# Optimization experiments

Measured on AMD Instinct MI355X. Metric: run time of the kernel, lower is better.

Reference implementation:

```python
import jax, jax.numpy as jnp
import numpy as np

N_ATOMS = 10000
N_EDGES = 200000
L_MAX = 2
K_L = [32, 24, 16]  # k_max_l = n_element_channels * n_max_l

# (l1, l2, L) in the original loop order (l1 outer, l2 inner, L ascending)
PAIRS = [(0,0,0),(0,1,1),(0,2,2),
         (1,0,1),(1,1,0),(1,1,1),(1,1,2),(1,2,1),(1,2,2),
         (2,0,2),(2,1,1),(2,1,2),(2,2,0),(2,2,1),(2,2,2)]
# concatenated input width -> k_max_l[L] per (L, sigma) channel
LIN = {'0_1': (72, 32), '1_1': (80, 24), '1_m1': (40, 24), '2_1': (72, 16), '2_m1': (32, 16)}


def setup_inputs() -> dict:
    key = jax.random.key(0)
    it = iter(jax.random.split(key, 64))
    def nrm(shape):
        return jax.random.normal(next(it), shape, dtype=jnp.float32)
    inp = {}
    for l in range(L_MAX + 1):
        inp['rb%d' % l] = nrm((N_EDGES, K_L[l]))           # radial basis per l
    for l in range(L_MAX + 1):
        inp['sh%d' % l] = nrm((N_EDGES, 2*l+1, 1))         # spherical harmonics per l
    inp['emb'] = nrm((N_ATOMS, 1, K_L[0]))                 # initial center embedding
    for l in range(L_MAX + 1):
        inp['f%d' % l] = nrm((N_ATOMS, 2*l+1, K_L[l]))     # nu=1 equivariant features
    for (l1, l2, L) in PAIRS:
        inp['cg_%d_%d_%d' % (l1, l2, L)] = nrm(((2*l1+1)*(2*l2+1), 2*L+1))
    for LS, (fin, fout) in LIN.items():
        inp['W_' + LS] = nrm((fin, fout)) / np.float32(np.sqrt(fin))
        inp['b_' + LS] = nrm((fout,)) * 0.01
    inp['centers'] = jax.random.randint(next(it), (N_EDGES,), 0, N_ATOMS)
    inp['neighbors'] = jax.random.randint(next(it), (N_EDGES,), 0, N_ATOMS)
    inp['n_atoms'] = N_ATOMS
    return inp


def _normalize(x, dims):
    # Normalizer(dims): RMS normalization over the given dims
    return x * jax.lax.rsqrt(jnp.mean(x * x, axis=dims, keepdims=True) + 1e-12)


def _forward(floats, centers, neighbors, n_atoms):
    (rb0, rb1, rb2, sh0, sh1, sh2, emb, f0, f1, f2,
     cg_0_0_0, cg_0_1_1, cg_0_2_2, cg_1_0_1, cg_1_1_0, cg_1_1_1, cg_1_1_2,
     cg_1_2_1, cg_1_2_2, cg_2_0_2, cg_2_1_1, cg_2_1_2, cg_2_2_0, cg_2_2_1,
     cg_2_2_2, W_0_1, b_0_1, W_1_1, b_1_1, W_1_m1, b_1_m1, W_2_1, b_2_1,
     W_2_m1, b_2_m1) = floats
    rb = [rb0, rb1, rb2]; sh = [sh0, sh1, sh2]; feats = [f0, f1, f2]
    cgs = {'0_0_0': cg_0_0_0, '0_1_1': cg_0_1_1, '0_2_2': cg_0_2_2,
           '1_0_1': cg_1_0_1, '1_1_0': cg_1_1_0, '1_1_1': cg_1_1_1,
           '1_1_2': cg_1_1_2, '1_2_1': cg_1_2_1, '1_2_2': cg_1_2_2,
           '2_0_2': cg_2_0_2, '2_1_1': cg_2_1_1, '2_1_2': cg_2_1_2,
           '2_2_0': cg_2_2_0, '2_2_1': cg_2_2_1, '2_2_2': cg_2_2_2}
    lin = {'0_1': (W_0_1, b_0_1), '1_1': (W_1_1, b_1_1), '1_m1': (W_1_m1, b_1_m1),
           '2_1': (W_2_1, b_2_1), '2_m1': (W_2_m1, b_2_m1)}

    # ---- InvariantMessagePasser: density_l = scatter_add over centers of
    #      sh_l * rb_l * emb[neighbors]
    emb_n = emb[neighbors]                                       # [E, 1, k0]
    densities = []
    for l in range(L_MAX + 1):
        msg = sh[l] * rb[l][:, None, :] * emb_n[:, :, :K_L[l]]   # [E, 2l+1, k_l]
        densities.append(jax.ops.segment_sum(msg, centers, num_segments=n_atoms))

    # ---- EquivariantMessagePasser
    ve = [sh[l] * rb[l][:, None, :] for l in range(L_MAX + 1)]   # vector expansion [E,2l+1,k_l]
    fn = [feats[l][neighbors] for l in range(L_MAX + 1)]         # gathered neighbor feats
    results = {}
    for (l1, l2, L) in PAIRS:
        S = (-1) ** (l1 + l2 + L)
        k = min(K_L[l1], K_L[l2])
        t1 = ve[l1][:, :, :k]                                    # [E, 2l1+1, k]
        t2 = fn[l2][:, :, :k]                                    # [E, 2l2+1, k]
        cg = cgs['%d_%d_%d' % (l1, l2, L)].reshape(2*l1+1, 2*l2+1, 2*L+1)
        # fused outer product + CG contraction -> [E, 2L+1, k]
        res = jnp.einsum('eak,ebk,abM->eMk', t1, t2, cg)
        pooled = jax.ops.segment_sum(res, centers, num_segments=n_atoms)
        LS = '%d_%s' % (L, 'm1' if S < 0 else '1')
        results.setdefault(LS, []).append(pooled)

    outs = {}
    for LS, (W, b) in lin.items():
        x = jnp.concatenate(results[LS], axis=2)                 # [n_atoms, 2L+1, size_LS]
        x = _normalize(x, (0, 1))
        x = jnp.einsum('amf,fk->amk', x, W) + b
        outs[LS] = _normalize(x, (0, 1, 2))

    return (densities[0], densities[1], densities[2],
            outs['0_1'], outs['1_1'], outs['1_m1'], outs['2_1'], outs['2_m1'])


def reference(rb0, rb1, rb2, sh0, sh1, sh2, emb, f0, f1, f2,
              cg_0_0_0, cg_0_1_1, cg_0_2_2, cg_1_0_1, cg_1_1_0, cg_1_1_1,
              cg_1_1_2, cg_1_2_1, cg_1_2_2, cg_2_0_2, cg_2_1_1, cg_2_1_2,
              cg_2_2_0, cg_2_2_1, cg_2_2_2, W_0_1, b_0_1, W_1_1, b_1_1,
              W_1_m1, b_1_m1, W_2_1, b_2_1, W_2_m1, b_2_m1,
              centers, neighbors, n_atoms):
    floats = (rb0, rb1, rb2, sh0, sh1, sh2, emb, f0, f1, f2,
              cg_0_0_0, cg_0_1_1, cg_0_2_2, cg_1_0_1, cg_1_1_0, cg_1_1_1,
              cg_1_1_2, cg_1_2_1, cg_1_2_2, cg_2_0_2, cg_2_1_1, cg_2_1_2,
              cg_2_2_0, cg_2_2_1, cg_2_2_2, W_0_1, b_0_1, W_1_1, b_1_1,
              W_1_m1, b_1_m1, W_2_1, b_2_1, W_2_m1, b_2_m1)
    return _forward(floats, centers, neighbors, n_atoms)
```

## Files before the change

### kernel.cpp

```cpp
#include <hip/hip_runtime.h>
#include <hip/hip_bf16.h>

typedef __hip_bfloat16 bf16;

#define N_ATOMS 10000
#define N_EDGES 200000

#define SCG   0
#define SINV  616
#define SS1P  1024
#define SS2P  19968
#define SWS2  20288
#define SINTS 20352
#define IFLAG  0
#define ICOUNT 16
#define IOFFS  10016
#define ICURS  20032
#define IELIST 30032
#define INTS_END_SMALL 230032
#define INTS_END_BIG   430032
#define SXACC (SINTS + INTS_END_BIG)
#define BIG_FLOATS (SXACC + 952*N_ATOMS)

#define O0 0
#define O1 320000
#define O2 1040000
#define OY 1840000
#define OUT_ELEMS 5200000

__device__ __forceinline__ float b2f(bf16 x){ return __bfloat162float(x); }
__device__ __forceinline__ bf16  f2b(float x){ return __float2bfloat16(x); }

__device__ __forceinline__ float ldv(const float* p, int i){ return p[i]; }
__device__ __forceinline__ float ldv(const bf16*  p, int i){ return b2f(p[i]); }
__device__ __forceinline__ void  stv(float* p, int i, float v){ p[i] = v; }
__device__ __forceinline__ void  stv(bf16*  p, int i, float v){ p[i] = f2b(v); }

template<typename T> __device__ __forceinline__ int dtid();
template<> __device__ __forceinline__ int dtid<bf16>(){ return 0; }
template<> __device__ __forceinline__ int dtid<float>(){ return 1; }

struct Ptrs15 { const void* p[15]; };
struct LinP   { const void* W[5]; const void* B[5]; };

__constant__ int c_cg_sizes[15] = {1,9,25,9,9,27,45,45,75,25,45,75,25,75,125};
__constant__ int c_fin[5]   = {72,80,40,72,32};
__constant__ int c_kout[5]  = {32,24,24,16,16};
__constant__ int c_yoff[5]  = {OY+0, OY+320000, OY+1040000, OY+1760000, OY+2560000};
__constant__ int c_numel[5] = {320000,720000,720000,800000,800000};
__constant__ int c_cum[6]   = {0,32,104,176,256,336};
__constant__ int c_xb[5]    = {0,72,312,432,792};
__constant__ int c_Ms[5]    = {1,3,3,5,5};

__global__ void k_zero(float* wsf, int* wsi,
                       const unsigned short* rb0u, const unsigned short* embu) {
  if (blockIdx.x == 0 && threadIdx.x < 64) {
    int lane = threadIdx.x;
    int bad = 0;
    for (int i = lane; i < 256; i += 64) {
      unsigned u1 = ((unsigned)rb0u[2*i]) << 16;
      unsigned u2 = ((unsigned)embu[2*i]) << 16;
      float v1 = __uint_as_float(u1);
      float v2 = __uint_as_float(u2);
      if (!(fabsf(v1) < 1e9f) || !(fabsf(v2) < 1e9f)) bad = 1;
    }
    unsigned long long any = __ballot(bad);
    if (lane == 0) wsi[IFLAG] = (any != 0ULL) ? 1 : 0;
  }
  int i = blockIdx.x*blockDim.x + threadIdx.x;
  if (i < N_ATOMS) wsi[ICOUNT + i] = 0;
  int j = i - N_ATOMS;
  if (j >= 0 && j < N_ATOMS) wsi[ICURS + j] = 0;
  j -= N_ATOMS;
  if (j >= 0 && j < 18944) wsf[SS1P + j] = 0.f;
  j -= 18944;
  if (j >= 0 && j < 325) wsf[SS2P + j] = 0.f;
}

template<typename T>
__global__ void k_cg(Ptrs15 cg, float* wsf, const int* flag) {
  if (flag[0] != dtid<T>()) return;
  int i = blockIdx.x*blockDim.x + threadIdx.x;
  if (i >= 615) return;
  int s = 0, off = i;
  while (off >= c_cg_sizes[s]) { off -= c_cg_sizes[s]; ++s; }
  wsf[SCG + i] = ldv((const T*)cg.p[s], off);
}

__global__ void k_hist(const int* __restrict__ centers, int* __restrict__ counts) {
  int e = blockIdx.x*blockDim.x + threadIdx.x;
  if (e < N_EDGES) atomicAdd(&counts[centers[e]], 1);
}

__global__ void k_scan(const int* __restrict__ counts, int* __restrict__ offs) {
  __shared__ int part[1024];
  int t = threadIdx.x;
  int base = t*10;
  int s = 0;
  for (int i = 0; i < 10; ++i) { int idx = base+i; if (idx < N_ATOMS) s += counts[idx]; }
  part[t] = s;
  __syncthreads();
  for (int d = 1; d < 1024; d <<= 1) {
    int v = part[t];
    int add = (t >= d) ? part[t-d] : 0;
    __syncthreads();
    part[t] = v + add;
    __syncthreads();
  }
  int run = (t == 0) ? 0 : part[t-1];
  for (int i = 0; i < 10; ++i) {
    int idx = base+i;
    if (idx < N_ATOMS) { offs[idx] = run; run += counts[idx]; }
  }
  if (t == 1023) offs[N_ATOMS] = part[1023];
}

__global__ void k_scatter(const int* __restrict__ centers, const int* __restrict__ offs,
                          int* __restrict__ cursors, int* __restrict__ elist) {
  int e = blockIdx.x*blockDim.x + threadIdx.x;
  if (e < N_EDGES) {
    int c = centers[e];
    int p = atomicAdd(&cursors[c], 1);
    elist[offs[c] + p] = e;
  }
}

__global__ void k_scatter2(const int* __restrict__ centers, const int* __restrict__ neighbors,
                           const int* __restrict__ offs, int* __restrict__ cursors,
                           int2* __restrict__ elist2) {
  int e = blockIdx.x*blockDim.x + threadIdx.x;
  if (e < N_EDGES) {
    int c = centers[e];
    int p = atomicAdd(&cursors[c], 1);
    elist2[offs[c] + p] = make_int2(e, neighbors[e]);
  }
}

template<typename T, int MODE>
__global__ __launch_bounds__(256) void k_main(
    const T* __restrict__ rb0, const T* __restrict__ rb1, const T* __restrict__ rb2,
    const T* __restrict__ sh0, const T* __restrict__ sh1, const T* __restrict__ sh2,
    const T* __restrict__ emb, const T* __restrict__ f0, const T* __restrict__ f1,
    const T* __restrict__ f2, const int* __restrict__ neighbors,
    const int* __restrict__ offs, const int* __restrict__ elist,
    const float* __restrict__ cgf, float* __restrict__ s1p,
    const float* __restrict__ inv, float* __restrict__ s2p,
    float* __restrict__ xout, LinP lp, T* __restrict__ out,
    const int* __restrict__ flag)
{
  if (flag[0] != dtid<T>()) return;
  int lane = threadIdx.x & 63;
  int wv   = threadIdx.x >> 6;
  int tix  = threadIdx.x;
  int a = blockIdx.x;
  int beg = offs[a];
  int cnt = offs[a+1] - beg;
  int k32 = lane & 31, e2 = lane >> 5;
  int k16 = lane & 15, e4 = lane >> 4;
  const int2* el2 = (const int2*)elist;
  int ab = a & 63;

  __shared__ int2 sel[256];
  __shared__ __align__(16) float L[952];
  __shared__ float red[4][5];

  float acc[25];
  #pragma unroll
  for (int i = 0; i < 25; ++i) acc[i] = 0.f;

  for (int cbase = 0; cbase < cnt; cbase += 256) {
    int nch = cnt - cbase; if (nch > 256) nch = 256;
    __syncthreads();
    if (tix < nch) {
      if constexpr (MODE == 0) {
        sel[tix] = el2[beg + cbase + tix];
      } else {
        int e = elist[beg + cbase + tix];
        sel[tix] = make_int2(e, neighbors[e]);
      }
    }
    __syncthreads();

    if (wv == 0) {
      for (int base = 0; base < nch; base += 4) {
        #pragma unroll
        for (int u = 0; u < 2; ++u) {
          int idx = base + 2*u + e2;
          float w = (idx < nch) ? 1.f : 0.f;
          int ic  = (idx < nch) ? idx : 0;
          int2 en = sel[ic];
          int e = en.x, n = en.y;
          float s0 = ldv(sh0, e);
          float s1a0 = ldv(sh1, e*3+0), s1a1 = ldv(sh1, e*3+1), s1a2 = ldv(sh1, e*3+2);
          float rb0k = ldv(rb0, e*32 + k32) * w;
          float ek   = ldv(emb, n*32 + k32);
          float f0k  = ldv(f0,  n*32 + k32);
          float ve0 = s0 * rb0k;
          acc[0] = fmaf(ve0, ek, acc[0]);
          acc[4] = fmaf(ve0, f0k, acc[4]);
          if (k32 < 24) {
            float rb1k = ldv(rb1, e*24 + k32) * w;
            float f1k0 = ldv(f1, n*72 + k32);
            float f1k1 = ldv(f1, n*72 + 24 + k32);
            float f1k2 = ldv(f1, n*72 + 48 + k32);
            float rbek = rb1k * ek;
            acc[1] = fmaf(s1a0, rbek, acc[1]);
            acc[2] = fmaf(s1a1, rbek, acc[2]);
            acc[3] = fmaf(s1a2, rbek, acc[3]);
            acc[5] = fmaf(ve0, f1k0, acc[5]);
            acc[6] = fmaf(ve0, f1k1, acc[6]);
            acc[7] = fmaf(ve0, f1k2, acc[7]);
            float g3 = rb1k * f0k;
            acc[8]  = fmaf(g3, s1a0, acc[8]);
            acc[9]  = fmaf(g3, s1a1, acc[9]);
            acc[10] = fmaf(g3, s1a2, acc[10]);
            #pragma unroll
            for (int aa = 0; aa < 3; ++aa) {
              float sa = rb1k * ((aa==0)?s1a0:(aa==1)?s1a1:s1a2);
              acc[11+aa*3+0] = fmaf(sa, f1k0, acc[11+aa*3+0]);
              acc[11+aa*3+1] = fmaf(sa, f1k1, acc[11+aa*3+1]);
              acc[11+aa*3+2] = fmaf(sa, f1k2, acc[11+aa*3+2]);
            }
          }
        }
      }
    } else if (wv == 1) {
      for (int base = 0; base < nch; base += 8) {
        #pragma unroll
        for (int u = 0; u < 2; ++u) {
          int idx = base + 4*u + e4;
          float w = (idx < nch) ? 1.f : 0.f;
          int ic  = (idx < nch) ? idx : 0;
          int2 en = sel[ic];
          int e = en.x, n = en.y;
          float s0 = ldv(sh0, e);
          float s1a[3];
          #pragma unroll
          for (int m = 0; m < 3; ++m) s1a[m] = ldv(sh1, e*3+m);
          float s2a[5];
          #pragma unroll
          for (int m = 0; m < 5; ++m) s2a[m] = ldv(sh2, e*5+m);
          float rb0k = ldv(rb0, e*32 + k16) * w;
          float rb1k = ldv(rb1, e*24 + k16) * w;
          float rb2k = ldv(rb2, e*16 + k16) * w;
          float ek   = ldv(emb, n*32 + k16);
          float f2k[5];
          #pragma unroll
          for (int b = 0; b < 5; ++b) f2k[b] = ldv(f2, n*80 + b*16 + k16);
          float re = rb2k * ek;
          #pragma unroll
          for (int m = 0; m < 5; ++m) acc[m] = fmaf(s2a[m], re, acc[m]);
          float ve0 = s0 * rb0k;
          #pragma unroll
          for (int b = 0; b < 5; ++b) acc[5+b] = fmaf(ve0, f2k[b], acc[5+b]);
          #pragma unroll
          for (int aa = 0; aa < 3; ++aa) {
            float sa = rb1k * s1a[aa];
            #pragma unroll
            for (int b = 0; b < 5; ++b)
              acc[10+aa*5+b] = fmaf(sa, f2k[b], acc[10+aa*5+b]);
          }
        }
      }
    } else if (wv == 2) {
      for (int base = 0; base < nch; base += 8) {
        #pragma unroll
        for (int u = 0; u < 2; ++u) {
          int idx = base + 4*u + e4;
          float w = (idx < nch) ? 1.f : 0.f;
          int ic  = (idx < nch) ? idx : 0;
          int2 en = sel[ic];
          int e = en.x, n = en.y;
          float s2a[5];
          #pragma unroll
          for (int m = 0; m < 5; ++m) s2a[m] = ldv(sh2, e*5+m);
          float rb2k = ldv(rb2, e*16 + k16) * w;
          float f0k  = ldv(f0,  n*32 + k16);
          float f1k[3];
          #pragma unroll
          for (int b = 0; b < 3; ++b) f1k[b] = ldv(f1, n*72 + b*24 + k16);
          float g9 = rb2k * f0k;
          #pragma unroll
          for (int aa = 0; aa < 5; ++aa) acc[aa] = fmaf(g9, s2a[aa], acc[aa]);
          #pragma unroll
          for (int aa = 0; aa < 5; ++aa) {
            float sa = rb2k * s2a[aa];
            #pragma unroll
            for (int b = 0; b < 3; ++b)
              acc[5+aa*3+b] = fmaf(sa, f1k[b], acc[5+aa*3+b]);
          }
        }
      }
    } else {
      for (int base = 0; base < nch; base += 8) {
        #pragma unroll
        for (int u = 0; u < 2; ++u) {
          int idx = base + 4*u + e4;
          float w = (idx < nch) ? 1.f : 0.f;
          int ic  = (idx < nch) ? idx : 0;
          int2 en = sel[ic];
          int e = en.x, n = en.y;
          float s2a[5];
          #pragma unroll
          for (int m = 0; m < 5; ++m) s2a[m] = ldv(sh2, e*5+m);
          float rb2k = ldv(rb2, e*16 + k16) * w;
          float f2k[5];
          #pragma unroll
          for (int b = 0; b < 5; ++b) f2k[b] = ldv(f2, n*80 + b*16 + k16);
          #pragma unroll
          for (int aa = 0; aa < 5; ++aa) {
            float sa = rb2k * s2a[aa];
            #pragma unroll
            for (int b = 0; b < 5; ++b)
              acc[aa*5+b] = fmaf(sa, f2k[b], acc[aa*5+b]);
          }
        }
      }
    }
  }

  if (wv == 0) {
    #pragma unroll
    for (int i = 0; i < 20; ++i) acc[i] += __shfl_xor(acc[i], 32);
    const float* C000 = cgf + 0;
    const float* C011 = cgf + 1;
    const float* C101 = cgf + 35;
    const float* C110 = cgf + 44;
    const float* C111 = cgf + 53;
    const float* C112 = cgf + 80;
    float r[16];
    r[0] = C000[0] * acc[4];
    #pragma unroll
    for (int M = 0; M < 3; ++M) {
      float t = 0.f;
      #pragma unroll
      for (int b = 0; b < 3; ++b) t = fmaf(acc[5+b], C011[b*3+M], t);
      r[1+M] = t;
    }
    #pragma unroll
    for (int M = 0; M < 3; ++M) {
      float t = 0.f;
      #pragma unroll
      for (int aa = 0; aa < 3; ++aa) t = fmaf(acc[8+aa], C101[aa*3+M], t);
      r[4+M] = t;
    }
    {
      float t = 0.f;
      #pragma unroll
      for (int q = 0; q < 9; ++q) t = fmaf(acc[11+q], C110[q], t);
      r[7] = t;
    }
    #pragma unroll
    for (int M = 0; M < 3; ++M) {
      float t = 0.f;
      #pragma unroll
      for (int q = 0; q < 9; ++q) t = fmaf(acc[11+q], C111[q*3+M], t);
      r[8+M] = t;
    }
    #pragma unroll
    for (int M = 0; M < 5; ++M) {
      float t = 0.f;
      #pragma unroll
      for (int q = 0; q < 9; ++q) t = fmaf(acc[11+q], C112[q*5+M], t);
      r[11+M] = t;
    }
    acc[4] = r[0];
    #pragma unroll
    for (int M = 0; M < 3; ++M) acc[5+M]  = r[1+M];
    #pragma unroll
    for (int M = 0; M < 3; ++M) acc[8+M]  = r[4+M];
    acc[11] = r[7];
    #pragma unroll
    for (int M = 0; M < 3; ++M) acc[12+M] = r[8+M];
    #pragma unroll
    for (int M = 0; M < 5; ++M) acc[15+M] = r[11+M];
  } else if (wv == 1) {
    #pragma unroll
    for (int i = 0; i < 25; ++i) {
      acc[i] += __shfl_xor(acc[i], 16);
      acc[i] += __shfl_xor(acc[i], 32);
    }
    const float* C022 = cgf + 10;
    const float* C121 = cgf + 125;
    const float* C122 = cgf + 170;
    float r[13];
    #pragma unroll
    for (int M = 0; M < 5; ++M) {
      float t = 0.f;
      #pragma unroll
      for (int b = 0; b < 5; ++b) t = fmaf(acc[5+b], C022[b*5+M], t);
      r[M] = t;
    }
    #pragma unroll
    for (int M = 0; M < 3; ++M) {
      float t = 0.f;
      #pragma unroll
      for (int q = 0; q < 15; ++q) t = fmaf(acc[10+q], C121[q*3+M], t);
      r[5+M] = t;
    }
    #pragma unroll
    for (int M = 0; M < 5; ++M) {
      float t = 0.f;
      #pragma unroll
      for (int q = 0; q < 15; ++q) t = fmaf(acc[10+q], C122[q*5+M], t);
      r[8+M] = t;
    }
    #pragma unroll
    for (int M = 0; M < 5; ++M) acc[5+M]  = r[M];
    #pragma unroll
    for (int M = 0; M < 3; ++M) acc[10+M] = r[5+M];
    #pragma unroll
    for (int M = 0; M < 5; ++M) acc[13+M] = r[8+M];
  } else if (wv == 2) {
    #pragma unroll
    for (int i = 0; i < 20; ++i) {
      acc[i] += __shfl_xor(acc[i], 16);
      acc[i] += __shfl_xor(acc[i], 32);
    }
    const float* C202 = cgf + 245;
    const float* C211 = cgf + 270;
    const float* C212 = cgf + 315;
    float r[13];
    #pragma unroll
    for (int M = 0; M < 5; ++M) {
      float t = 0.f;
      #pragma unroll
      for (int aa = 0; aa < 5; ++aa) t = fmaf(acc[aa], C202[aa*5+M], t);
      r[M] = t;
    }
    #pragma unroll
    for (int M = 0; M < 3; ++M) {
      float t = 0.f;
      #pragma unroll
      for (int q = 0; q < 15; ++q) t = fmaf(acc[5+q], C211[q*3+M], t);
      r[5+M] = t;
    }
    #pragma unroll
    for (int M = 0; M < 5; ++M) {
      float t = 0.f;
      #pragma unroll
      for (int q = 0; q < 15; ++q) t = fmaf(acc[5+q], C212[q*5+M], t);
      r[8+M] = t;
    }
    #pragma unroll
    for (int M = 0; M < 5; ++M) acc[M]   = r[M];
    #pragma unroll
    for (int M = 0; M < 3; ++M) acc[5+M] = r[5+M];
    #pragma unroll
    for (int M = 0; M < 5; ++M) acc[8+M] = r[8+M];
  } else {
    #pragma unroll
    for (int i = 0; i < 25; ++i) {
      acc[i] += __shfl_xor(acc[i], 16);
      acc[i] += __shfl_xor(acc[i], 32);
    }
    const float* C220 = cgf + 390;
    const float* C221 = cgf + 415;
    const float* C222 = cgf + 490;
    float r[9];
    {
      float t = 0.f;
      #pragma unroll
      for (int q = 0; q < 25; ++q) t = fmaf(acc[q], C220[q], t);
      r[0] = t;
    }
    #pragma unroll
    for (int M = 0; M < 3; ++M) {
      float t = 0.f;
      #pragma unroll
      for (int q = 0; q < 25; ++q) t = fmaf(acc[q], C221[q*3+M], t);
      r[1+M] = t;
    }
    #pragma unroll
    for (int M = 0; M < 5; ++M) {
      float t = 0.f;
      #pragma unroll
      for (int q = 0; q < 25; ++q) t = fmaf(acc[q], C222[q*5+M], t);
      r[4+M] = t;
    }
    #pragma unroll
    for (int i = 0; i < 9; ++i) acc[i] = r[i];
  }

  if constexpr (MODE != 2) {
    if (wv == 0) {
      if (lane < 32) {
        stv(out, O0 + a*32 + k32, acc[0]);
        atomicAdd(&s1p[(0+k32)*64+ab], acc[4]*acc[4]);
        if (k32 < 24) {
          #pragma unroll
          for (int m = 0; m < 3; ++m) stv(out, O1 + a*72 + m*24 + k32, acc[1+m]);
          atomicAdd(&s1p[(32+k32)*64+ab], acc[11]*acc[11]);
          float q;
          q = acc[5]*acc[5]+acc[6]*acc[6]+acc[7]*acc[7];
          atomicAdd(&s1p[(72+k32)*64+ab], q);
          q = acc[8]*acc[8]+acc[9]*acc[9]+acc[10]*acc[10];
          atomicAdd(&s1p[(96+k32)*64+ab], q);
          q = acc[12]*acc[12]+acc[13]*acc[13]+acc[14]*acc[14];
          atomicAdd(&s1p[(152+k32)*64+ab], q);
          q = acc[15]*acc[15]+acc[16]*acc[16]+acc[17]*acc[17]
            + acc[18]*acc[18]+acc[19]*acc[19];
          atomicAdd(&s1p[(208+k32)*64+ab], q);
        }
      }
    } else if (wv == 1) {
      if (lane < 16) {
        #pragma unroll
        for (int m = 0; m < 5; ++m) stv(out, O2 + a*80 + m*16 + k16, acc[m]);
        float q;
        q = acc[5]*acc[5]+acc[6]*acc[6]+acc[7]*acc[7]+acc[8]*acc[8]+acc[9]*acc[9];
        atomicAdd(&s1p[(192+k16)*64+ab], q);
        q = acc[10]*acc[10]+acc[11]*acc[11]+acc[12]*acc[12];
        atomicAdd(&s1p[(120+k16)*64+ab], q);
        q = acc[13]*acc[13]+acc[14]*acc[14]+acc[15]*acc[15]
          + acc[16]*acc[16]+acc[17]*acc[17];
        atomicAdd(&s1p[(264+k16)*64+ab], q);
      }
    } else if (wv == 2) {
      if (lane < 16) {
        float q;
        q = acc[0]*acc[0]+acc[1]*acc[1]+acc[2]*acc[2]+acc[3]*acc[3]+acc[4]*acc[4];
        atomicAdd(&s1p[(232+k16)*64+ab], q);
        q = acc[5]*acc[5]+acc[6]*acc[6]+acc[7]*acc[7];
        atomicAdd(&s1p[(136+k16)*64+ab], q);
        q = acc[8]*acc[8]+acc[9]*acc[9]+acc[10]*acc[10]
          + acc[11]*acc[11]+acc[12]*acc[12];
        atomicAdd(&s1p[(280+k16)*64+ab], q);
      }
    } else {
      if (lane < 16) {
        atomicAdd(&s1p[(56+k16)*64+ab], acc[0]*acc[0]);
        float q;
        q = acc[1]*acc[1]+acc[2]*acc[2]+acc[3]*acc[3];
        atomicAdd(&s1p[(176+k16)*64+ab], q);
        q = acc[4]*acc[4]+acc[5]*acc[5]+acc[6]*acc[6]
          + acc[7]*acc[7]+acc[8]*acc[8];
        atomicAdd(&s1p[(248+k16)*64+ab], q);
      }
    }
  }

  if constexpr (MODE == 0) {
    if (wv == 0) {
      if (lane < 32) {
        L[k32] = acc[4];
        if (k32 < 24) {
          L[32+k32] = acc[11];
          #pragma unroll
          for (int M = 0; M < 3; ++M) L[72+M*80+k32]     = acc[5+M];
          #pragma unroll
          for (int M = 0; M < 3; ++M) L[72+M*80+24+k32]  = acc[8+M];
          #pragma unroll
          for (int M = 0; M < 3; ++M) L[312+M*40+k32]    = acc[12+M];
          #pragma unroll
          for (int M = 0; M < 5; ++M) L[432+M*72+16+k32] = acc[15+M];
        }
      }
    } else if (wv == 1) {
      if (lane < 16) {
        #pragma unroll
        for (int M = 0; M < 5; ++M) L[432+M*72+k16]    = acc[5+M];
        #pragma unroll
        for (int M = 0; M < 3; ++M) L[72+M*80+48+k16]  = acc[10+M];
        #pragma unroll
        for (int M = 0; M < 5; ++M) L[792+M*32+k16]    = acc[13+M];
      }
    } else if (wv == 2) {
      if (lane < 16) {
        #pragma unroll
        for (int M = 0; M < 5; ++M) L[432+M*72+40+k16] = acc[0+M];
        #pragma unroll
        for (int M = 0; M < 3; ++M) L[72+M*80+64+k16]  = acc[5+M];
        #pragma unroll
        for (int M = 0; M < 5; ++M) L[792+M*32+16+k16] = acc[8+M];
      }
    } else {
      if (lane < 16) {
        L[56+k16] = acc[0];
        #pragma unroll
        for (int M = 0; M < 3; ++M) L[312+M*40+24+k16] = acc[1+M];
        #pragma unroll
        for (int M = 0; M < 5; ++M) L[432+M*72+56+k16] = acc[4+M];
      }
    }
    __syncthreads();
    const float4* Ls = (const float4*)L;
    float4* xd = (float4*)(xout + a*952);
    for (int i = tix; i < 238; i += 256) xd[i] = Ls[i];
  }

  if constexpr (MODE == 2) {
    if (wv == 0) {
      if (lane < 32) {
        L[k32] = acc[4]*inv[k32];
        if (k32 < 24) {
          L[32+k32] = acc[11]*inv[32+k32];
          #pragma unroll
          for (int M = 0; M < 3; ++M) L[72+M*80+k32]     = acc[5+M]*inv[72+k32];
          #pragma unroll
          for (int M = 0; M < 3; ++M) L[72+M*80+24+k32]  = acc[8+M]*inv[96+k32];
          #pragma unroll
          for (int M = 0; M < 3; ++M) L[312+M*40+k32]    = acc[12+M]*inv[152+k32];
          #pragma unroll
          for (int M = 0; M < 5; ++M) L[432+M*72+16+k32] = acc[15+M]*inv[208+k32];
        }
      }
    } else if (wv == 1) {
      if (lane < 16) {
        #pragma unroll
        for (int M = 0; M < 5; ++M) L[432+M*72+k16]    = acc[5+M]*inv[192+k16];
        #pragma unroll
        for (int M = 0; M < 3; ++M) L[72+M*80+48+k16]  = acc[10+M]*inv[120+k16];
        #pragma unroll
        for (int M = 0; M < 5; ++M) L[792+M*32+k16]    = acc[13+M]*inv[264+k16];
      }
    } else if (wv == 2) {
      if (lane < 16) {
        #pragma unroll
        for (int M = 0; M < 5; ++M) L[432+M*72+40+k16] = acc[0+M]*inv[232+k16];
        #pragma unroll
        for (int M = 0; M < 3; ++M) L[72+M*80+64+k16]  = acc[5+M]*inv[136+k16];
        #pragma unroll
        for (int M = 0; M < 5; ++M) L[792+M*32+16+k16] = acc[8+M]*inv[280+k16];
      }
    } else {
      if (lane < 16) {
        L[56+k16] = acc[0]*inv[56+k16];
        #pragma unroll
        for (int M = 0; M < 3; ++M) L[312+M*40+24+k16] = acc[1+M]*inv[176+k16];
        #pragma unroll
        for (int M = 0; M < 5; ++M) L[432+M*72+56+k16] = acc[4+M]*inv[248+k16];
      }
    }
    __syncthreads();
    int t = threadIdx.x;
    float y2[5] = {0.f,0.f,0.f,0.f,0.f};
    for (int tau = t; tau < 336; tau += 256) {
      int ls = 0;
      while (tau >= c_cum[ls+1]) ++ls;
      int rem = tau - c_cum[ls];
      int kn = c_kout[ls], fin = c_fin[ls];
      int M = rem / kn, ko = rem - M*kn;
      const T* W = (const T*)lp.W[ls];
      float y = ldv((const T*)lp.B[ls], ko);
      const float* xv = &L[c_xb[ls] + M*fin];
      for (int f = 0; f < fin; ++f) y = fmaf(xv[f], ldv(W, f*kn+ko), y);
      stv(out, c_yoff[ls] + (a*c_Ms[ls] + M)*kn + ko, y);
      y2[ls] += y*y;
    }
    #pragma unroll
    for (int i = 0; i < 5; ++i) {
      y2[i] += __shfl_xor(y2[i], 1);  y2[i] += __shfl_xor(y2[i], 2);
      y2[i] += __shfl_xor(y2[i], 4);  y2[i] += __shfl_xor(y2[i], 8);
      y2[i] += __shfl_xor(y2[i], 16); y2[i] += __shfl_xor(y2[i], 32);
    }
    if (lane == 0) {
      #pragma unroll
      for (int i = 0; i < 5; ++i) red[wv][i] = y2[i];
    }
    __syncthreads();
    if (t == 0) {
      #pragma unroll
      for (int i = 0; i < 5; ++i)
        atomicAdd(&s2p[i*64 + ab], red[0][i]+red[1][i]+red[2][i]+red[3][i]);
    }
  }
}

template<typename T>
__global__ __launch_bounds__(256) void k_lin(
    const float* __restrict__ xg, const float* __restrict__ inv,
    LinP lp, T* __restrict__ out, float* __restrict__ s2p,
    const int* __restrict__ flag)
{
  if (flag[0] != dtid<T>()) return;
  int a = blockIdx.x;
  int t = threadIdx.x;
  __shared__ float L[952];
  for (int i = t; i < 952; i += 256) {
    int ch;
    if      (i < 72)  ch = i;
    else if (i < 312) ch = 72  + (i-72)  % 80;
    else if (i < 432) ch = 152 + (i-312) % 40;
    else if (i < 792) ch = 192 + (i-432) % 72;
    else              ch = 264 + (i-792) % 32;
    L[i] = xg[a*952 + i] * inv[ch];
  }
  __syncthreads();
  float y2[5] = {0.f,0.f,0.f,0.f,0.f};
  for (int tau = t; tau < 336; tau += 256) {
    int ls = 0;
    while (tau >= c_cum[ls+1]) ++ls;
    int rem = tau - c_cum[ls];
    int kn = c_kout[ls], fin = c_fin[ls];
    int M = rem / kn, ko = rem - M*kn;
    const T* W = (const T*)lp.W[ls];
    float y = ldv((const T*)lp.B[ls], ko);
    const float* xv = &L[c_xb[ls] + M*fin];
    for (int f = 0; f < fin; ++f) y = fmaf(xv[f], ldv(W, f*kn+ko), y);
    stv(out, c_yoff[ls] + (a*c_Ms[ls] + M)*kn + ko, y);
    y2[ls] += y*y;
  }
  __shared__ float red[4][5];
  #pragma unroll
  for (int i = 0; i < 5; ++i) {
    y2[i] += __shfl_xor(y2[i], 1);  y2[i] += __shfl_xor(y2[i], 2);
    y2[i] += __shfl_xor(y2[i], 4);  y2[i] += __shfl_xor(y2[i], 8);
    y2[i] += __shfl_xor(y2[i], 16); y2[i] += __shfl_xor(y2[i], 32);
  }
  if ((t & 63) == 0) {
    #pragma unroll
    for (int i = 0; i < 5; ++i) red[t>>6][i] = y2[i];
  }
  __syncthreads();
  if (t == 0) {
    #pragma unroll
    for (int i = 0; i < 5; ++i)
      atomicAdd(&s2p[i*64 + (a & 63)], red[0][i]+red[1][i]+red[2][i]+red[3][i]);
  }
}

__global__ void k_red1(const float* __restrict__ s1p, float* __restrict__ inv) {
  int ch = blockIdx.x, lane = threadIdx.x;
  float v = s1p[ch*64 + lane];
  v += __shfl_xor(v, 1);  v += __shfl_xor(v, 2);  v += __shfl_xor(v, 4);
  v += __shfl_xor(v, 8);  v += __shfl_xor(v, 16); v += __shfl_xor(v, 32);
  if (lane == 0) {
    float rows = (ch < 72) ? 10000.f : (ch < 192) ? 30000.f : 50000.f;
    inv[ch] = rsqrtf(v/rows + 1e-12f);
  }
}

__global__ void k_red2(const float* __restrict__ s2p, float* __restrict__ ws2) {
  int ls = blockIdx.x, lane = threadIdx.x;
  float v = s2p[ls*64 + lane];
  v += __shfl_xor(v, 1);  v += __shfl_xor(v, 2);  v += __shfl_xor(v, 4);
  v += __shfl_xor(v, 8);  v += __shfl_xor(v, 16); v += __shfl_xor(v, 32);
  if (lane == 0) ws2[ls] = v;
}

template<typename T>
__global__ void k_scale(const float* __restrict__ ws2, T* __restrict__ out,
                        const int* __restrict__ flag) {
  if (flag[0] != dtid<T>()) return;
  int i = blockIdx.x*blockDim.x + threadIdx.x;
  if (i >= 3360000) return;
  int ls = (i < 320000) ? 0 : (i < 1040000) ? 1 : (i < 1760000) ? 2 : (i < 2560000) ? 3 : 4;
  float scale = rsqrtf(ws2[ls] / (float)c_numel[ls] + 1e-12f);
  stv(out, OY + i, ldv((const T*)out, OY + i) * scale);
}

template<typename T>
static void launch_chain(void* const* d_in, T* out, float* wsf, int* wsi,
                         Ptrs15 cg, LinP lp, bool big, hipStream_t stream) {
  const T* rb0 = (const T*)d_in[0];
  const T* rb1 = (const T*)d_in[1];
  const T* rb2 = (const T*)d_in[2];
  const T* sh0 = (const T*)d_in[3];
  const T* sh1 = (const T*)d_in[4];
  const T* sh2 = (const T*)d_in[5];
  const T* emb = (const T*)d_in[6];
  const T* f0  = (const T*)d_in[7];
  const T* f1  = (const T*)d_in[8];
  const T* f2  = (const T*)d_in[9];
  const int* neighbors = (const int*)d_in[36];
  const int* flag = wsi + IFLAG;

  k_cg<T><<<3, 256, 0, stream>>>(cg, wsf, flag);
  if (big) {
    k_main<T,0><<<N_ATOMS, 256, 0, stream>>>(rb0, rb1, rb2, sh0, sh1, sh2, emb, f0, f1, f2,
        neighbors, wsi+IOFFS, wsi+IELIST, wsf+SCG, wsf+SS1P, nullptr, nullptr,
        wsf+SXACC, lp, out, flag);
    k_red1<<<296, 64, 0, stream>>>(wsf+SS1P, wsf+SINV);
    k_lin<T><<<N_ATOMS, 256, 0, stream>>>(wsf+SXACC, wsf+SINV, lp, out, wsf+SS2P, flag);
  } else {
    k_main<T,1><<<N_ATOMS, 256, 0, stream>>>(rb0, rb1, rb2, sh0, sh1, sh2, emb, f0, f1, f2,
        neighbors, wsi+IOFFS, wsi+IELIST, wsf+SCG, wsf+SS1P, nullptr, nullptr,
        nullptr, lp, out, flag);
    k_red1<<<296, 64, 0, stream>>>(wsf+SS1P, wsf+SINV);
    k_main<T,2><<<N_ATOMS, 256, 0, stream>>>(rb0, rb1, rb2, sh0, sh1, sh2, emb, f0, f1, f2,
        neighbors, wsi+IOFFS, wsi+IELIST, wsf+SCG, nullptr, wsf+SINV, wsf+SS2P,
        nullptr, lp, out, flag);
  }
  k_red2<<<5, 64, 0, stream>>>(wsf+SS2P, wsf+SWS2);
  k_scale<T><<<(3360000+255)/256, 256, 0, stream>>>(wsf+SWS2, out, flag);
}

extern "C" void kernel_launch(void* const* d_in, const int* in_sizes, int n_in,
                              void* d_out, int out_size, void* d_ws, size_t ws_size,
                              hipStream_t stream) {
  float* wsf = (float*)d_ws;
  int*   wsi = (int*)(wsf + SINTS);
  const int* centers   = (const int*)d_in[35];
  const int* neighbors = (const int*)d_in[36];
  bool big = ws_size >= (size_t)BIG_FLOATS * 4;

  int know = -1;
  if (in_sizes) {
    long long nb = (long long)in_sizes[0];
    if (nb == (long long)N_EDGES*32*2) know = 0;
    else if (nb == (long long)N_EDGES*32*4) know = 1;
  }
  if (know < 0) {
    long long ob = (long long)out_size;
    if (ob == (long long)OUT_ELEMS*2) know = 0;
    else if (ob == (long long)OUT_ELEMS*4) know = 1;
  }

  Ptrs15 cg;
  for (int i = 0; i < 15; ++i) cg.p[i] = d_in[10+i];
  LinP lp;
  lp.W[0] = d_in[25]; lp.B[0] = d_in[26];
  lp.W[1] = d_in[27]; lp.B[1] = d_in[28];
  lp.W[2] = d_in[29]; lp.B[2] = d_in[30];
  lp.W[3] = d_in[31]; lp.B[3] = d_in[32];
  lp.W[4] = d_in[33]; lp.B[4] = d_in[34];

  k_zero<<<154, 256, 0, stream>>>(wsf, wsi,
                                  (const unsigned short*)d_in[0],
                                  (const unsigned short*)d_in[6]);
  k_hist<<<(N_EDGES+255)/256, 256, 0, stream>>>(centers, wsi+ICOUNT);
  k_scan<<<1, 1024, 0, stream>>>(wsi+ICOUNT, wsi+IOFFS);
  if (big) {
    k_scatter2<<<(N_EDGES+255)/256, 256, 0, stream>>>(centers, neighbors, wsi+IOFFS,
                                                      wsi+ICURS, (int2*)(wsi+IELIST));
  } else {
    k_scatter<<<(N_EDGES+255)/256, 256, 0, stream>>>(centers, wsi+IOFFS, wsi+ICURS, wsi+IELIST);
  }

  if (know != 1) launch_chain<bf16 >(d_in, (bf16*)d_out,  wsf, wsi, cg, lp, big, stream);
  if (know != 0) launch_chain<float>(d_in, (float*)d_out, wsf, wsi, cg, lp, big, stream);
}
```

Measured before the change: 514.2 us.

## Stage per-edge and neighbor rows into shared memory with vectorized loads

Each block now processes edges in chunks of 32 and cooperatively copies each edge's radial basis and spherical harmonics, plus the neighbor's embedding and feature rows, into shared memory using 4-wide vector loads. The four wave-specialized loops then read from shared memory instead of issuing scattered scalar global loads per lane, and the same rows are no longer fetched separately by every wave. The int2 edge list and its scatter2 kernel are dropped, so the neighbor index is always looked up at chunk load. In exchange there are more block barriers per atom (every 32 edges instead of 256), a larger shared-memory footprint that may cut occupancy, and the v4 casts assume 16-byte (float) or 8-byte (bf16) alignment of the row offsets.

```diff
diff --git a/kernel.cpp b/kernel.cpp
--- a/kernel.cpp
+++ b/kernel.cpp
@@ -17,9 +17,8 @@
 #define IOFFS  10016
 #define ICURS  20032
 #define IELIST 30032
-#define INTS_END_SMALL 230032
-#define INTS_END_BIG   430032
-#define SXACC (SINTS + INTS_END_BIG)
+#define INTS_END 230032
+#define SXACC (SINTS + INTS_END)
 #define BIG_FLOATS (SXACC + 952*N_ATOMS)
 
 #define O0 0
@@ -35,6 +34,13 @@
 __device__ __forceinline__ float ldv(const bf16*  p, int i){ return b2f(p[i]); }
 __device__ __forceinline__ void  stv(float* p, int i, float v){ p[i] = v; }
 __device__ __forceinline__ void  stv(bf16*  p, int i, float v){ p[i] = f2b(v); }
+
+__device__ __forceinline__ void v4cp(bf16* d, const bf16* s){
+  *reinterpret_cast<ushort4*>(d) = *reinterpret_cast<const ushort4*>(s);
+}
+__device__ __forceinline__ void v4cp(float* d, const float* s){
+  *reinterpret_cast<float4*>(d) = *reinterpret_cast<const float4*>(s);
+}
 
 template<typename T> __device__ __forceinline__ int dtid();
 template<> __device__ __forceinline__ int dtid<bf16>(){ return 0; }
@@ -122,17 +128,6 @@
     int c = centers[e];
     int p = atomicAdd(&cursors[c], 1);
     elist[offs[c] + p] = e;
-  }
-}
-
-__global__ void k_scatter2(const int* __restrict__ centers, const int* __restrict__ neighbors,
-                           const int* __restrict__ offs, int* __restrict__ cursors,
-                           int2* __restrict__ elist2) {
-  int e = blockIdx.x*blockDim.x + threadIdx.x;
-  if (e < N_EDGES) {
-    int c = centers[e];
-    int p = atomicAdd(&cursors[c], 1);
-    elist2[offs[c] + p] = make_int2(e, neighbors[e]);
   }
 }
 
@@ -157,10 +152,11 @@
   int cnt = offs[a+1] - beg;
   int k32 = lane & 31, e2 = lane >> 5;
   int k16 = lane & 15, e4 = lane >> 4;
-  const int2* el2 = (const int2*)elist;
   int ab = a & 63;
 
-  __shared__ int2 sel[256];
+  __shared__ int2 sel[32];
+  __shared__ T SE[32][84];
+  __shared__ T SN[32][216];
   __shared__ __align__(16) float L[952];
   __shared__ float red[4][5];
 
@@ -168,15 +164,37 @@
   #pragma unroll
   for (int i = 0; i < 25; ++i) acc[i] = 0.f;
 
-  for (int cbase = 0; cbase < cnt; cbase += 256) {
-    int nch = cnt - cbase; if (nch > 256) nch = 256;
+  for (int cbase = 0; cbase < cnt; cbase += 32) {
+    int nch = cnt - cbase; if (nch > 32) nch = 32;
     __syncthreads();
     if (tix < nch) {
-      if constexpr (MODE == 0) {
-        sel[tix] = el2[beg + cbase + tix];
-      } else {
-        int e = elist[beg + cbase + tix];
-        sel[tix] = make_int2(e, neighbors[e]);
+      int e = elist[beg + cbase + tix];
+      sel[tix] = make_int2(e, neighbors[e]);
+    }
+    __syncthreads();
+    {
+      int i = tix >> 3, p = tix & 7;
+      if (i < nch) {
+        int e = sel[i].x, n = sel[i].y;
+        v4cp(&SE[i][p*4], rb0 + e*32 + p*4);
+        if (p < 6) v4cp(&SE[i][32 + p*4], rb1 + e*24 + p*4);
+        if (p < 4) v4cp(&SE[i][56 + p*4], rb2 + e*16 + p*4);
+        if (p == 0) { SE[i][72] = sh0[e]; SE[i][80] = sh2[e*5+4]; }
+        else if (p < 4) SE[i][72+p] = sh1[e*3 + p-1];
+        else            SE[i][72+p] = sh2[e*5 + p-4];
+        #pragma unroll
+        for (int uu = 0; uu < 7; ++uu) {
+          int g = p + uu*8;
+          if (g < 54) {
+            int ch = g*4;
+            const T* src; int off;
+            if (ch < 32)       { src = emb; off = n*32 + ch; }
+            else if (ch < 64)  { src = f0;  off = n*32 + ch - 32; }
+            else if (ch < 136) { src = f1;  off = n*72 + ch - 64; }
+            else               { src = f2;  off = n*80 + ch - 136; }
+            v4cp(&SN[i][ch], src + off);
+          }
+        }
       }
     }
     __syncthreads();
@@ -188,21 +206,21 @@
           int idx = base + 2*u + e2;
           float w = (idx < nch) ? 1.f : 0.f;
           int ic  = (idx < nch) ? idx : 0;
-          int2 en = sel[ic];
-          int e = en.x, n = en.y;
-          float s0 = ldv(sh0, e);
-          float s1a0 = ldv(sh1, e*3+0), s1a1 = ldv(sh1, e*3+1), s1a2 = ldv(sh1, e*3+2);
-          float rb0k = ldv(rb0, e*32 + k32) * w;
-          float ek   = ldv(emb, n*32 + k32);
-          float f0k  = ldv(f0,  n*32 + k32);
+          const T* rE = SE[ic];
+          const T* rN = SN[ic];
+          float s0 = ldv(rE,72);
+          float s1a0 = ldv(rE,73), s1a1 = ldv(rE,74), s1a2 = ldv(rE,75);
+          float rb0k = ldv(rE, k32) * w;
+          float ek   = ldv(rN, k32);
+          float f0k  = ldv(rN, 32+k32);
           float ve0 = s0 * rb0k;
           acc[0] = fmaf(ve0, ek, acc[0]);
           acc[4] = fmaf(ve0, f0k, acc[4]);
           if (k32 < 24) {
-            float rb1k = ldv(rb1, e*24 + k32) * w;
-            float f1k0 = ldv(f1, n*72 + k32);
-            float f1k1 = ldv(f1, n*72 + 24 + k32);
-            float f1k2 = ldv(f1, n*72 + 48 + k32);
+            float rb1k = ldv(rE, 32+k32) * w;
+            float f1k0 = ldv(rN, 64+k32);
+            float f1k1 = ldv(rN, 64+24+k32);
+            float f1k2 = ldv(rN, 64+48+k32);
             float rbek = rb1k * ek;
             acc[1] = fmaf(s1a0, rbek, acc[1]);
             acc[2] = fmaf(s1a1, rbek, acc[2]);
@@ -231,22 +249,22 @@
           int idx = base + 4*u + e4;
           float w = (idx < nch) ? 1.f : 0.f;
           int ic  = (idx < nch) ? idx : 0;
-          int2 en = sel[ic];
-          int e = en.x, n = en.y;
-          float s0 = ldv(sh0, e);
+          const T* rE = SE[ic];
+          const T* rN = SN[ic];
+          float s0 = ldv(rE,72);
           float s1a[3];
           #pragma unroll
-          for (int m = 0; m < 3; ++m) s1a[m] = ldv(sh1, e*3+m);
+          for (int m = 0; m < 3; ++m) s1a[m] = ldv(rE, 73+m);
           float s2a[5];
           #pragma unroll
-          for (int m = 0; m < 5; ++m) s2a[m] = ldv(sh2, e*5+m);
-          float rb0k = ldv(rb0, e*32 + k16) * w;
-          float rb1k = ldv(rb1, e*24 + k16) * w;
-          float rb2k = ldv(rb2, e*16 + k16) * w;
-          float ek   = ldv(emb, n*32 + k16);
+          for (int m = 0; m < 5; ++m) s2a[m] = ldv(rE, 76+m);
+          float rb0k = ldv(rE, k16) * w;
+          float rb1k = ldv(rE, 32+k16) * w;
+          float rb2k = ldv(rE, 56+k16) * w;
+          float ek   = ldv(rN, k16);
           float f2k[5];
           #pragma unroll
-          for (int b = 0; b < 5; ++b) f2k[b] = ldv(f2, n*80 + b*16 + k16);
+          for (int b = 0; b < 5; ++b) f2k[b] = ldv(rN, 136 + b*16 + k16);
           float re = rb2k * ek;
           #pragma unroll
           for (int m = 0; m < 5; ++m) acc[m] = fmaf(s2a[m], re, acc[m]);
@@ -269,16 +287,16 @@
           int idx = base + 4*u + e4;
           float w = (idx < nch) ? 1.f : 0.f;
           int ic  = (idx < nch) ? idx : 0;
-          int2 en = sel[ic];
-          int e = en.x, n = en.y;
+          const T* rE = SE[ic];
+          const T* rN = SN[ic];
           float s2a[5];
           #pragma unroll
-          for (int m = 0; m < 5; ++m) s2a[m] = ldv(sh2, e*5+m);
-          float rb2k = ldv(rb2, e*16 + k16) * w;
-          float f0k  = ldv(f0,  n*32 + k16);
+          for (int m = 0; m < 5; ++m) s2a[m] = ldv(rE, 76+m);
+          float rb2k = ldv(rE, 56+k16) * w;
+          float f0k  = ldv(rN, 32+k16);
           float f1k[3];
           #pragma unroll
-          for (int b = 0; b < 3; ++b) f1k[b] = ldv(f1, n*72 + b*24 + k16);
+          for (int b = 0; b < 3; ++b) f1k[b] = ldv(rN, 64 + b*24 + k16);
           float g9 = rb2k * f0k;
           #pragma unroll
           for (int aa = 0; aa < 5; ++aa) acc[aa] = fmaf(g9, s2a[aa], acc[aa]);
@@ -298,15 +316,15 @@
           int idx = base + 4*u + e4;
           float w = (idx < nch) ? 1.f : 0.f;
           int ic  = (idx < nch) ? idx : 0;
-          int2 en = sel[ic];
-          int e = en.x, n = en.y;
+          const T* rE = SE[ic];
+          const T* rN = SN[ic];
           float s2a[5];
           #pragma unroll
-          for (int m = 0; m < 5; ++m) s2a[m] = ldv(sh2, e*5+m);
-          float rb2k = ldv(rb2, e*16 + k16) * w;
+          for (int m = 0; m < 5; ++m) s2a[m] = ldv(rE, 76+m);
+          float rb2k = ldv(rE, 56+k16) * w;
           float f2k[5];
           #pragma unroll
-          for (int b = 0; b < 5; ++b) f2k[b] = ldv(f2, n*80 + b*16 + k16);
+          for (int b = 0; b < 5; ++b) f2k[b] = ldv(rN, 136 + b*16 + k16);
           #pragma unroll
           for (int aa = 0; aa < 5; ++aa) {
             float sa = rb2k * s2a[aa];
@@ -792,7 +810,6 @@
   float* wsf = (float*)d_ws;
   int*   wsi = (int*)(wsf + SINTS);
   const int* centers   = (const int*)d_in[35];
-  const int* neighbors = (const int*)d_in[36];
   bool big = ws_size >= (size_t)BIG_FLOATS * 4;
 
   int know = -1;
@@ -821,12 +838,7 @@
                                   (const unsigned short*)d_in[6]);
   k_hist<<<(N_EDGES+255)/256, 256, 0, stream>>>(centers, wsi+ICOUNT);
   k_scan<<<1, 1024, 0, stream>>>(wsi+ICOUNT, wsi+IOFFS);
-  if (big) {
-    k_scatter2<<<(N_EDGES+255)/256, 256, 0, stream>>>(centers, neighbors, wsi+IOFFS,
-                                                      wsi+ICURS, (int2*)(wsi+IELIST));
-  } else {
-    k_scatter<<<(N_EDGES+255)/256, 256, 0, stream>>>(centers, wsi+IOFFS, wsi+ICURS, wsi+IELIST);
-  }
+  k_scatter<<<(N_EDGES+255)/256, 256, 0, stream>>>(centers, wsi+IOFFS, wsi+ICURS, wsi+IELIST);
 
   if (know != 1) launch_chain<bf16 >(d_in, (bf16*)d_out,  wsf, wsi, cg, lp, big, stream);
   if (know != 0) launch_chain<float>(d_in, (float*)d_out, wsf, wsi, cg, lp, big, stream);
```

Result: no change. 516.8 us (+0.5%).
